# Optimization experiments

Hardware: AMD Instinct MI355X
Metric: run time of the kernel (lower is better)

The kernel has to match this reference:

```python
import jax, jax.numpy as jnp
import numpy as np

LR = 0.001  # fixed self.lr in ODE_Vanilla

B, T, I, H, C = 128, 256, 256, 1024, 10


def setup_inputs() -> dict:
    key = jax.random.key(0)
    ks = jax.random.split(key, 6)
    stdv = 1.0 / np.sqrt(H)
    u = lambda k, shape: jax.random.uniform(k, shape, jnp.float32, -stdv, stdv)
    return {
        "X": jax.random.normal(ks[0], (B, T, I), jnp.float32),
        "hidden": jnp.zeros((B, H), jnp.float32),
        "alpha": jnp.zeros((1,), jnp.float32),  # alpha is excluded from re-init, stays 0.0
        "b": u(ks[1], (H,)),
        "Wh": u(ks[2], (H, H)),
        "Wx": u(ks[3], (I, H)),
        "fc_w": u(ks[4], (H, C)),
        "fc_b": u(ks[5], (C,)),
    }


def reference(X, hidden, alpha, b, Wh, Wx, fc_w, fc_b):
    # X: (B, T, I) -> scan over time-major (T, B, I)
    a = alpha[0]
    Xt = jnp.transpose(X, (1, 0, 2))

    def step(h, x):
        # phi = relu(h @ Wh + x @ Wx + b)
        phi = jax.nn.relu(h @ Wh + x @ Wx + b)
        mask = (phi > 0).astype(h.dtype)
        # st = a*I - diag(mask) @ Wh; grad = st @ (a*h - phi)
        # collapses to: a*v - mask * (v @ Wh^T), with v = a*h - phi
        v = a * h - phi
        grad = a * v - mask * (v @ Wh.T)
        h_new = h - LR * grad
        return h_new, h_new

    h_final, outs = jax.lax.scan(step, hidden, Xt)  # outs: (T, B, H)
    # last_layer (single_output=False, class task): FC over all timesteps
    out = jnp.transpose(outs, (1, 0, 2)) @ fc_w + fc_b  # (B, T, C)
    return out.reshape(-1, out.shape[-1]), h_final
```

## Files before the change

### kernel.cpp

```cpp
#include <hip/hip_runtime.h>


constexpr int Bsz = 128, Tn = 256, In = 256, Hn = 1024, Cn = 10;
constexpr float LR = 0.001f;

__global__ __launch_bounds__(256) void k_transpose(const float* __restrict__ W,
                                                   float* __restrict__ WT) {
  __shared__ float tile[32][33];
  const int bx = blockIdx.x * 32, by = blockIdx.y * 32;
  const int tx = threadIdx.x & 31, ty = threadIdx.x >> 5;
#pragma unroll
  for (int dy = 0; dy < 32; dy += 8)
    tile[ty + dy][tx] = W[(size_t)(by + ty + dy) * Hn + bx + tx];
  __syncthreads();
#pragma unroll
  for (int dy = 0; dy < 32; dy += 8)
    WT[(size_t)(bx + ty + dy) * Hn + by + tx] = tile[tx][ty + dy];
}

__global__ __launch_bounds__(256) void k_init(float* __restrict__ out,
                                              const float* __restrict__ fc_b,
                                              float* __restrict__ h_cur,
                                              const float* __restrict__ hidden) {
  const int i = blockIdx.x * blockDim.x + threadIdx.x;
  if (i < Bsz * Tn * Cn) out[i] = fc_b[i % Cn];
  if (i < Bsz * Hn) h_cur[i] = hidden[i];
}

__device__ __forceinline__ void fma4(float4& a, float s, const float4& w) {
  a.x = fmaf(s, w.x, a.x);
  a.y = fmaf(s, w.y, a.y);
  a.z = fmaf(s, w.z, a.z);
  a.w = fmaf(s, w.w, a.w);
}

__device__ __forceinline__ float4 shfl4(float4 v, int m) {
  v.x = __shfl_xor(v.x, m, 64);
  v.y = __shfl_xor(v.y, m, 64);
  v.z = __shfl_xor(v.z, m, 64);
  v.w = __shfl_xor(v.w, m, 64);
  return v;
}

__device__ __forceinline__ float4 add4(float4 a, float4 b) {
  return make_float4(a.x + b.x, a.y + b.y, a.z + b.z, a.w + b.w);
}

__global__ __launch_bounds__(256) void k_xw(const float* __restrict__ X,
                                            const float* __restrict__ Wx,
                                            const float* __restrict__ bias,
                                            float* __restrict__ xw) {
  const int nt = blockIdx.x & 15, mt = blockIdx.x >> 4;
  const int t = mt >> 1, b0 = (mt & 1) * 64;
  const int cl = threadIdx.x & 15, rg = threadIdx.x >> 4;
  const int col = nt * 64 + cl * 4;
  const int row = b0 + rg * 4;
  float4 acc0 = {0, 0, 0, 0}, acc1 = {0, 0, 0, 0}, acc2 = {0, 0, 0, 0},
         acc3 = {0, 0, 0, 0};
  const size_t xstride = (size_t)Tn * In;
  const float* xp = X + ((size_t)row * Tn + t) * In;
  const float* wp = Wx + col;
#pragma unroll 2
  for (int k = 0; k < In; k += 4) {
    const float4 x0 = *(const float4*)(xp + k);
    const float4 x1 = *(const float4*)(xp + xstride + k);
    const float4 x2 = *(const float4*)(xp + 2 * xstride + k);
    const float4 x3 = *(const float4*)(xp + 3 * xstride + k);
    const float4 w0 = *(const float4*)(wp + (size_t)k * Hn);
    const float4 w1 = *(const float4*)(wp + (size_t)(k + 1) * Hn);
    const float4 w2 = *(const float4*)(wp + (size_t)(k + 2) * Hn);
    const float4 w3 = *(const float4*)(wp + (size_t)(k + 3) * Hn);
    fma4(acc0, x0.x, w0); fma4(acc0, x0.y, w1); fma4(acc0, x0.z, w2); fma4(acc0, x0.w, w3);
    fma4(acc1, x1.x, w0); fma4(acc1, x1.y, w1); fma4(acc1, x1.z, w2); fma4(acc1, x1.w, w3);
    fma4(acc2, x2.x, w0); fma4(acc2, x2.y, w1); fma4(acc2, x2.z, w2); fma4(acc2, x2.w, w3);
    fma4(acc3, x3.x, w0); fma4(acc3, x3.y, w1); fma4(acc3, x3.z, w2); fma4(acc3, x3.w, w3);
  }
  const float4 b4 = *(const float4*)(bias + col);
  float4 o[4] = {acc0, acc1, acc2, acc3};
#pragma unroll
  for (int i = 0; i < 4; i++) {
    float4 v = o[i];
    v.x += b4.x; v.y += b4.y; v.z += b4.z; v.w += b4.w;
    *(float4*)(xw + ((size_t)t * Bsz + row + i) * Hn + col) = v;
  }
}

__device__ __forceinline__ void gemm8g(const float* __restrict__ rows,
                                       const float* __restrict__ W, int kk,
                                       int col, float4 acc[8]) {
#pragma unroll
  for (int q = 0; q < 4; q++) {
    const int k = 4 * kk + 256 * q;
    const float* Wp = W + (size_t)k * Hn + col;
    const float4 w0 = *(const float4*)(Wp);
    const float4 w1 = *(const float4*)(Wp + Hn);
    const float4 w2 = *(const float4*)(Wp + 2 * Hn);
    const float4 w3 = *(const float4*)(Wp + 3 * Hn);
#pragma unroll
    for (int r = 0; r < 8; r++) {
      const float4 h4 = *(const float4*)(rows + (size_t)r * Hn + k);
      fma4(acc[r], h4.x, w0);
      fma4(acc[r], h4.y, w1);
      fma4(acc[r], h4.z, w2);
      fma4(acc[r], h4.w, w3);
    }
  }
}

__device__ __forceinline__ void reduce_vs(float4 acc[8], int c4, int ksw,
                                          int wv, float (*part)[8][16]) {
  const bool u1 = ksw & 1;
#pragma unroll
  for (int i = 0; i < 4; i++) {
    const float4 snd = u1 ? acc[i] : acc[i + 4];
    const float4 kp = u1 ? acc[i + 4] : acc[i];
    acc[i] = add4(kp, shfl4(snd, 4));
  }
  const bool u2 = ksw & 2;
#pragma unroll
  for (int i = 0; i < 2; i++) {
    const float4 snd = u2 ? acc[i] : acc[i + 2];
    const float4 kp = u2 ? acc[i + 2] : acc[i];
    acc[i] = add4(kp, shfl4(snd, 8));
  }
  const bool u3 = ksw & 4;
  {
    const float4 snd = u3 ? acc[0] : acc[1];
    const float4 kp = u3 ? acc[1] : acc[0];
    acc[0] = add4(kp, shfl4(snd, 16));
  }
  const bool u4 = ksw & 8;
  float sx = u4 ? acc[0].x : acc[0].z;
  float sy = u4 ? acc[0].y : acc[0].w;
  const float kx = u4 ? acc[0].z : acc[0].x;
  const float ky = u4 ? acc[0].w : acc[0].y;
  sx = __shfl_xor(sx, 32, 64);
  sy = __shfl_xor(sy, 32, 64);
  const int r_own = ((ksw & 1) << 2) | (ksw & 2) | ((ksw >> 2) & 1);
  const int c_own = 4 * c4 + (u4 ? 2 : 0);
  *(float2*)&part[wv][r_own][c_own] = make_float2(kx + sx, ky + sy);
}

template <int PRE>
__global__ __launch_bounds__(256, 4) void k_phase1(
    const float* __restrict__ h, const float* __restrict__ X,
    const float* __restrict__ Wh, const float* __restrict__ Wx,
    const float* __restrict__ bias, const float* __restrict__ alpha,
    const float* __restrict__ xw, float* __restrict__ v_out, int t) {
  __shared__ float part[4][8][16];
  const int ct = blockIdx.x & 63, rt = blockIdx.x >> 6;
  const int c0 = ct * 16, r0 = rt * 8;
  const int tid = threadIdx.x;
  const int c4 = tid & 3, kk = tid >> 2;
  const int col = c0 + 4 * c4;
  const int wv = tid >> 6, ksw = (tid & 63) >> 2;
  const float* hbase = h + (size_t)r0 * Hn;

  float4 acc[8];
#pragma unroll
  for (int r = 0; r < 8; r++) acc[r] = {0.f, 0.f, 0.f, 0.f};
  gemm8g(hbase, Wh, kk, col, acc);
  if (!PRE) {
    const int kx = 4 * kk;
    const float* Wp = Wx + (size_t)kx * Hn + col;
    const float4 w0 = *(const float4*)(Wp);
    const float4 w1 = *(const float4*)(Wp + Hn);
    const float4 w2 = *(const float4*)(Wp + 2 * Hn);
    const float4 w3 = *(const float4*)(Wp + 3 * Hn);
#pragma unroll
    for (int r = 0; r < 8; r++) {
      const float4 x4 =
          *(const float4*)(X + ((size_t)(r0 + r) * Tn + t) * In + kx);
      fma4(acc[r], x4.x, w0);
      fma4(acc[r], x4.y, w1);
      fma4(acc[r], x4.z, w2);
      fma4(acc[r], x4.w, w3);
    }
  }
  reduce_vs(acc, c4, ksw, wv, part);
  __syncthreads();
  if (tid < 128) {
    const int r = tid >> 4, c = tid & 15;
    const float u =
        part[0][r][c] + part[1][r][c] + part[2][r][c] + part[3][r][c];
    const float a1 =
        PRE ? xw[((size_t)t * Bsz + r0 + r) * Hn + c0 + c] : bias[c0 + c];
    const float av = alpha[0];
    const float hv = hbase[(size_t)r * Hn + c0 + c];
    v_out[(size_t)(r0 + r) * Hn + c0 + c] = av * hv - fmaxf(u + a1, 0.f);
  }
}

__global__ __launch_bounds__(256, 4) void k_phase2(
    float* __restrict__ h, const float* __restrict__ v_in,
    const float* __restrict__ WT, const float* __restrict__ alpha,
    const float* __restrict__ fc_w, float* __restrict__ out,
    float* __restrict__ hfin, int t, int last) {
  __shared__ float part[4][8][16];
  __shared__ float hn_s[8][16];
  const int ct = blockIdx.x & 63, rt = blockIdx.x >> 6;
  const int c0 = ct * 16, r0 = rt * 8;
  const int tid = threadIdx.x;
  const int c4 = tid & 3, kk = tid >> 2;
  const int col = c0 + 4 * c4;
  const int wv = tid >> 6, ksw = (tid & 63) >> 2;
  const float* vbase = v_in + (size_t)r0 * Hn;

  float4 acc[8];
#pragma unroll
  for (int r = 0; r < 8; r++) acc[r] = {0.f, 0.f, 0.f, 0.f};
  gemm8g(vbase, WT, kk, col, acc);
  reduce_vs(acc, c4, ksw, wv, part);
  __syncthreads();
  if (tid < 128) {
    const int r = tid >> 4, c = tid & 15;
    const float u =
        part[0][r][c] + part[1][r][c] + part[2][r][c] + part[3][r][c];
    const float av = alpha[0];
    const size_t hoff = (size_t)(r0 + r) * Hn + c0 + c;
    const float vv = vbase[(size_t)r * Hn + c0 + c];
    const float hv = h[hoff];
    const float hn = hv - LR * (av * vv - ((av * hv - vv) > 0.f ? u : 0.f));
    h[hoff] = hn;
    if (last) hfin[hoff] = hn;
    hn_s[r][c] = hn;
  }
  __syncthreads();
  if (tid < 80) {
    const int rr = tid / 10, c = tid % 10;
    float s = 0.f;
#pragma unroll
    for (int jj = 0; jj < 16; jj++)
      s += hn_s[rr][jj] * fc_w[(size_t)(c0 + jj) * Cn + c];
    atomicAdd(&out[((size_t)(r0 + rr) * Tn + t) * Cn + c], s);
  }
}

extern "C" void kernel_launch(void* const* d_in, const int* in_sizes, int n_in,
                              void* d_out, int out_size, void* d_ws, size_t ws_size,
                              hipStream_t stream) {
  const float* X      = (const float*)d_in[0];
  const float* hidden = (const float*)d_in[1];
  const float* alpha  = (const float*)d_in[2];
  const float* bias   = (const float*)d_in[3];
  const float* Wh     = (const float*)d_in[4];
  const float* Wx     = (const float*)d_in[5];
  const float* fc_w   = (const float*)d_in[6];
  const float* fc_b   = (const float*)d_in[7];
  float* out  = (float*)d_out;
  float* hfin = out + (size_t)Bsz * Tn * Cn;

  char* ws = (char*)d_ws;
  float* WhT   = (float*)ws;
  float* h_cur = WhT + (size_t)Hn * Hn;
  float* v_buf = h_cur + (size_t)Bsz * Hn;
  float* XW    = v_buf + (size_t)Bsz * Hn;
  const size_t need =
      ((size_t)Hn * Hn + 2 * (size_t)Bsz * Hn + (size_t)Bsz * Tn * Hn) *
      sizeof(float);
  const bool pre = ws_size >= need;

  k_transpose<<<dim3(32, 32), 256, 0, stream>>>(Wh, WhT);
  k_init<<<(Bsz * Tn * Cn + 255) / 256, 256, 0, stream>>>(out, fc_b, h_cur,
                                                          hidden);
  if (pre) k_xw<<<8192, 256, 0, stream>>>(X, Wx, bias, XW);
  for (int t = 0; t < Tn; t++) {
    if (pre)
      k_phase1<1><<<1024, 256, 0, stream>>>(h_cur, X, Wh, Wx, bias, alpha, XW,
                                            v_buf, t);
    else
      k_phase1<0><<<1024, 256, 0, stream>>>(h_cur, X, Wh, Wx, bias, alpha, XW,
                                            v_buf, t);
    k_phase2<<<1024, 256, 0, stream>>>(h_cur, v_buf, WhT, alpha, fc_w, out,
                                       hfin, t, t == Tn - 1);
  }
}
```

Baseline: 6.030 ms.

## Move FC projection into extra phase1 blocks for previous timestep, drop atomics

The per-timestep FC output projection is removed from the tail of phase2, where it added a sync and atomicAdds. It now runs in 16 extra blocks of the next step's phase1 launch, which read the previous h_cur and write the output directly with the bias added. A final small kernel handles the last timestep, and the init kernel no longer fills the output with the bias. This shortens phase2's critical path and removes atomic contention, at the cost of some imbalance from the extra phase1 blocks.

```diff
diff --git a/kernel.cpp b/kernel.cpp
--- a/kernel.cpp
+++ b/kernel.cpp
@@ -18,13 +18,10 @@
     WT[(size_t)(bx + ty + dy) * Hn + by + tx] = tile[tx][ty + dy];
 }
 
-__global__ __launch_bounds__(256) void k_init(float* __restrict__ out,
-                                              const float* __restrict__ fc_b,
-                                              float* __restrict__ h_cur,
+__global__ __launch_bounds__(256) void k_init(float* __restrict__ h_cur,
                                               const float* __restrict__ hidden) {
-  const int i = blockIdx.x * blockDim.x + threadIdx.x;
-  if (i < Bsz * Tn * Cn) out[i] = fc_b[i % Cn];
-  if (i < Bsz * Hn) h_cur[i] = hidden[i];
+  const int i = blockIdx.x * 256 + threadIdx.x;
+  h_cur[i] = hidden[i];
 }
 
 __device__ __forceinline__ void fma4(float4& a, float s, const float4& w) {
@@ -146,11 +143,36 @@
     const float* __restrict__ h, const float* __restrict__ X,
     const float* __restrict__ Wh, const float* __restrict__ Wx,
     const float* __restrict__ bias, const float* __restrict__ alpha,
-    const float* __restrict__ xw, float* __restrict__ v_out, int t) {
+    const float* __restrict__ xw, const float* __restrict__ fc_w,
+    const float* __restrict__ fc_b, float* __restrict__ out,
+    float* __restrict__ v_out, int t) {
+  const int tid = threadIdx.x;
+  if (blockIdx.x >= 1024) {
+    if (t == 0) return;
+    const int r0b = (blockIdx.x - 1024) * 8;
+    const int r = tid >> 5, l = tid & 31;
+    const int c = l & 15, half = l >> 4;
+    float s = 0.f;
+    if (c < Cn) {
+      const float* hp = h + (size_t)(r0b + r) * Hn + half * 512;
+#pragma unroll 4
+      for (int k = 0; k < 512; k += 4) {
+        const float4 h4 = *(const float4*)(hp + k);
+        const float* fw = fc_w + (size_t)(half * 512 + k) * Cn + c;
+        s = fmaf(h4.x, fw[0], s);
+        s = fmaf(h4.y, fw[Cn], s);
+        s = fmaf(h4.z, fw[2 * Cn], s);
+        s = fmaf(h4.w, fw[3 * Cn], s);
+      }
+    }
+    s += __shfl_xor(s, 16, 64);
+    if (c < Cn && half == 0)
+      out[((size_t)(r0b + r) * Tn + (t - 1)) * Cn + c] = s + fc_b[c];
+    return;
+  }
   __shared__ float part[4][8][16];
   const int ct = blockIdx.x & 63, rt = blockIdx.x >> 6;
   const int c0 = ct * 16, r0 = rt * 8;
-  const int tid = threadIdx.x;
   const int c4 = tid & 3, kk = tid >> 2;
   const int col = c0 + 4 * c4;
   const int wv = tid >> 6, ksw = (tid & 63) >> 2;
@@ -194,10 +216,8 @@
 __global__ __launch_bounds__(256, 4) void k_phase2(
     float* __restrict__ h, const float* __restrict__ v_in,
     const float* __restrict__ WT, const float* __restrict__ alpha,
-    const float* __restrict__ fc_w, float* __restrict__ out,
-    float* __restrict__ hfin, int t, int last) {
+    float* __restrict__ hfin, int last) {
   __shared__ float part[4][8][16];
-  __shared__ float hn_s[8][16];
   const int ct = blockIdx.x & 63, rt = blockIdx.x >> 6;
   const int c0 = ct * 16, r0 = rt * 8;
   const int tid = threadIdx.x;
@@ -223,17 +243,32 @@
     const float hn = hv - LR * (av * vv - ((av * hv - vv) > 0.f ? u : 0.f));
     h[hoff] = hn;
     if (last) hfin[hoff] = hn;
-    hn_s[r][c] = hn;
-  }
-  __syncthreads();
-  if (tid < 80) {
-    const int rr = tid / 10, c = tid % 10;
-    float s = 0.f;
-#pragma unroll
-    for (int jj = 0; jj < 16; jj++)
-      s += hn_s[rr][jj] * fc_w[(size_t)(c0 + jj) * Cn + c];
-    atomicAdd(&out[((size_t)(r0 + rr) * Tn + t) * Cn + c], s);
-  }
+  }
+}
+
+__global__ __launch_bounds__(256) void k_fc_last(const float* __restrict__ h,
+                                                 const float* __restrict__ fc_w,
+                                                 const float* __restrict__ fc_b,
+                                                 float* __restrict__ out) {
+  const int r0 = blockIdx.x * 8;
+  const int r = threadIdx.x >> 5, l = threadIdx.x & 31;
+  const int c = l & 15, half = l >> 4;
+  float s = 0.f;
+  if (c < Cn) {
+    const float* hp = h + (size_t)(r0 + r) * Hn + half * 512;
+#pragma unroll 4
+    for (int k = 0; k < 512; k += 4) {
+      const float4 h4 = *(const float4*)(hp + k);
+      const float* fw = fc_w + (size_t)(half * 512 + k) * Cn + c;
+      s = fmaf(h4.x, fw[0], s);
+      s = fmaf(h4.y, fw[Cn], s);
+      s = fmaf(h4.z, fw[2 * Cn], s);
+      s = fmaf(h4.w, fw[3 * Cn], s);
+    }
+  }
+  s += __shfl_xor(s, 16, 64);
+  if (c < Cn && half == 0)
+    out[((size_t)(r0 + r) * Tn + (Tn - 1)) * Cn + c] = s + fc_b[c];
 }
 
 extern "C" void kernel_launch(void* const* d_in, const int* in_sizes, int n_in,
@@ -261,17 +296,17 @@
   const bool pre = ws_size >= need;
 
   k_transpose<<<dim3(32, 32), 256, 0, stream>>>(Wh, WhT);
-  k_init<<<(Bsz * Tn * Cn + 255) / 256, 256, 0, stream>>>(out, fc_b, h_cur,
-                                                          hidden);
+  k_init<<<512, 256, 0, stream>>>(h_cur, hidden);
   if (pre) k_xw<<<8192, 256, 0, stream>>>(X, Wx, bias, XW);
   for (int t = 0; t < Tn; t++) {
     if (pre)
-      k_phase1<1><<<1024, 256, 0, stream>>>(h_cur, X, Wh, Wx, bias, alpha, XW,
-                                            v_buf, t);
+      k_phase1<1><<<1040, 256, 0, stream>>>(h_cur, X, Wh, Wx, bias, alpha, XW,
+                                            fc_w, fc_b, out, v_buf, t);
     else
-      k_phase1<0><<<1024, 256, 0, stream>>>(h_cur, X, Wh, Wx, bias, alpha, XW,
-                                            v_buf, t);
-    k_phase2<<<1024, 256, 0, stream>>>(h_cur, v_buf, WhT, alpha, fc_w, out,
-                                       hfin, t, t == Tn - 1);
-  }
-}
+      k_phase1<0><<<1040, 256, 0, stream>>>(h_cur, X, Wh, Wx, bias, alpha, XW,
+                                            fc_w, fc_b, out, v_buf, t);
+    k_phase2<<<1024, 256, 0, stream>>>(h_cur, v_buf, WhT, alpha, hfin,
+                                       t == Tn - 1);
+  }
+  k_fc_last<<<16, 256, 0, stream>>>(h_cur, fc_w, fc_b, out);
+}
```

After: 7.036 ms. +16.7%, slower.

## Enlarge recurrent GEMM tiles to 16 rows with 512-thread blocks

Applied to the files above, without the earlier changes.

Each per-step phase kernel now computes a 16-row by 16-column output tile with 512 threads instead of an 8x16 tile with 256 threads. Every weight float4 loaded is reused across twice as many batch rows, which halves total weight traffic per timestep and halves the block count. The cross-lane reduction is reworked to fit the larger accumulator array, and the epilogue loads of h, v and xw are hoisted above the GEMM so their latency overlaps it. In exchange, each thread holds 16 float4 accumulators, which raises register pressure and may lower occupancy. Only 512 blocks run per launch.

```diff
diff --git a/kernel.cpp b/kernel.cpp
--- a/kernel.cpp
+++ b/kernel.cpp
@@ -85,19 +85,19 @@
   }
 }
 
-__device__ __forceinline__ void gemm8g(const float* __restrict__ rows,
-                                       const float* __restrict__ W, int kk,
-                                       int col, float4 acc[8]) {
-#pragma unroll
-  for (int q = 0; q < 4; q++) {
-    const int k = 4 * kk + 256 * q;
+__device__ __forceinline__ void gemm16g(const float* __restrict__ rows,
+                                        const float* __restrict__ W, int kk,
+                                        int col, float4 acc[16]) {
+#pragma unroll
+  for (int q = 0; q < 2; q++) {
+    const int k = 4 * kk + 512 * q;
     const float* Wp = W + (size_t)k * Hn + col;
     const float4 w0 = *(const float4*)(Wp);
     const float4 w1 = *(const float4*)(Wp + Hn);
     const float4 w2 = *(const float4*)(Wp + 2 * Hn);
     const float4 w3 = *(const float4*)(Wp + 3 * Hn);
 #pragma unroll
-    for (int r = 0; r < 8; r++) {
+    for (int r = 0; r < 16; r++) {
       const float4 h4 = *(const float4*)(rows + (size_t)r * Hn + k);
       fma4(acc[r], h4.x, w0);
       fma4(acc[r], h4.y, w1);
@@ -107,126 +107,132 @@
   }
 }
 
-__device__ __forceinline__ void reduce_vs(float4 acc[8], int c4, int ksw,
-                                          int wv, float (*part)[8][16]) {
+__device__ __forceinline__ void reduce_vs16(float4 acc[16], int c4, int ksw,
+                                            int wv, float (*part)[16][20]) {
   const bool u1 = ksw & 1;
 #pragma unroll
+  for (int i = 0; i < 8; i++) {
+    const float4 snd = u1 ? acc[i] : acc[i + 8];
+    const float4 kp = u1 ? acc[i + 8] : acc[i];
+    acc[i] = add4(kp, shfl4(snd, 4));
+  }
+  const bool u2 = ksw & 2;
+#pragma unroll
   for (int i = 0; i < 4; i++) {
-    const float4 snd = u1 ? acc[i] : acc[i + 4];
-    const float4 kp = u1 ? acc[i + 4] : acc[i];
-    acc[i] = add4(kp, shfl4(snd, 4));
-  }
-  const bool u2 = ksw & 2;
+    const float4 snd = u2 ? acc[i] : acc[i + 4];
+    const float4 kp = u2 ? acc[i + 4] : acc[i];
+    acc[i] = add4(kp, shfl4(snd, 8));
+  }
+  const bool u3 = ksw & 4;
 #pragma unroll
   for (int i = 0; i < 2; i++) {
-    const float4 snd = u2 ? acc[i] : acc[i + 2];
-    const float4 kp = u2 ? acc[i + 2] : acc[i];
-    acc[i] = add4(kp, shfl4(snd, 8));
-  }
-  const bool u3 = ksw & 4;
+    const float4 snd = u3 ? acc[i] : acc[i + 2];
+    const float4 kp = u3 ? acc[i + 2] : acc[i];
+    acc[i] = add4(kp, shfl4(snd, 16));
+  }
+  const bool u4 = ksw & 8;
   {
-    const float4 snd = u3 ? acc[0] : acc[1];
-    const float4 kp = u3 ? acc[1] : acc[0];
-    acc[0] = add4(kp, shfl4(snd, 16));
-  }
-  const bool u4 = ksw & 8;
-  float sx = u4 ? acc[0].x : acc[0].z;
-  float sy = u4 ? acc[0].y : acc[0].w;
-  const float kx = u4 ? acc[0].z : acc[0].x;
-  const float ky = u4 ? acc[0].w : acc[0].y;
-  sx = __shfl_xor(sx, 32, 64);
-  sy = __shfl_xor(sy, 32, 64);
-  const int r_own = ((ksw & 1) << 2) | (ksw & 2) | ((ksw >> 2) & 1);
-  const int c_own = 4 * c4 + (u4 ? 2 : 0);
-  *(float2*)&part[wv][r_own][c_own] = make_float2(kx + sx, ky + sy);
+    const float4 snd = u4 ? acc[0] : acc[1];
+    const float4 kp = u4 ? acc[1] : acc[0];
+    acc[0] = add4(kp, shfl4(snd, 32));
+  }
+  const int r_own = (u1 ? 8 : 0) | (u2 ? 4 : 0) | (u3 ? 2 : 0) | (u4 ? 1 : 0);
+  *(float4*)&part[wv][r_own][4 * c4] = acc[0];
 }
 
 template <int PRE>
-__global__ __launch_bounds__(256, 4) void k_phase1(
+__global__ __launch_bounds__(512, 4) void k_phase1(
     const float* __restrict__ h, const float* __restrict__ X,
     const float* __restrict__ Wh, const float* __restrict__ Wx,
     const float* __restrict__ bias, const float* __restrict__ alpha,
     const float* __restrict__ xw, float* __restrict__ v_out, int t) {
-  __shared__ float part[4][8][16];
+  __shared__ float part[8][16][20];
   const int ct = blockIdx.x & 63, rt = blockIdx.x >> 6;
-  const int c0 = ct * 16, r0 = rt * 8;
+  const int c0 = ct * 16, r0 = rt * 16;
   const int tid = threadIdx.x;
   const int c4 = tid & 3, kk = tid >> 2;
   const int col = c0 + 4 * c4;
-  const int wv = tid >> 6, ksw = (tid & 63) >> 2;
+  const int wv = tid >> 6, ksw = (tid >> 2) & 15;
   const float* hbase = h + (size_t)r0 * Hn;
 
-  float4 acc[8];
-#pragma unroll
-  for (int r = 0; r < 8; r++) acc[r] = {0.f, 0.f, 0.f, 0.f};
-  gemm8g(hbase, Wh, kk, col, acc);
+  float a1 = 0.f, hv = 0.f;
+  if (tid < 256) {
+    const int r = tid >> 4, c = tid & 15;
+    a1 = PRE ? xw[((size_t)t * Bsz + r0 + r) * Hn + c0 + c] : bias[c0 + c];
+    hv = hbase[(size_t)r * Hn + c0 + c];
+  }
+
+  float4 acc[16];
+#pragma unroll
+  for (int r = 0; r < 16; r++) acc[r] = {0.f, 0.f, 0.f, 0.f};
+  gemm16g(hbase, Wh, kk, col, acc);
   if (!PRE) {
-    const int kx = 4 * kk;
+    const int kx = 2 * kk;
     const float* Wp = Wx + (size_t)kx * Hn + col;
-    const float4 w0 = *(const float4*)(Wp);
-    const float4 w1 = *(const float4*)(Wp + Hn);
-    const float4 w2 = *(const float4*)(Wp + 2 * Hn);
-    const float4 w3 = *(const float4*)(Wp + 3 * Hn);
-#pragma unroll
-    for (int r = 0; r < 8; r++) {
-      const float4 x4 =
-          *(const float4*)(X + ((size_t)(r0 + r) * Tn + t) * In + kx);
-      fma4(acc[r], x4.x, w0);
-      fma4(acc[r], x4.y, w1);
-      fma4(acc[r], x4.z, w2);
-      fma4(acc[r], x4.w, w3);
+    const float4 wa = *(const float4*)(Wp);
+    const float4 wb = *(const float4*)(Wp + Hn);
+#pragma unroll
+    for (int r = 0; r < 16; r++) {
+      const float2 x2 =
+          *(const float2*)(X + ((size_t)(r0 + r) * Tn + t) * In + kx);
+      fma4(acc[r], x2.x, wa);
+      fma4(acc[r], x2.y, wb);
     }
   }
-  reduce_vs(acc, c4, ksw, wv, part);
-  __syncthreads();
-  if (tid < 128) {
-    const int r = tid >> 4, c = tid & 15;
-    const float u =
-        part[0][r][c] + part[1][r][c] + part[2][r][c] + part[3][r][c];
-    const float a1 =
-        PRE ? xw[((size_t)t * Bsz + r0 + r) * Hn + c0 + c] : bias[c0 + c];
+  reduce_vs16(acc, c4, ksw, wv, part);
+  __syncthreads();
+  if (tid < 256) {
+    const int r = tid >> 4, c = tid & 15;
+    float u = part[0][r][c];
+#pragma unroll
+    for (int w = 1; w < 8; w++) u += part[w][r][c];
     const float av = alpha[0];
-    const float hv = hbase[(size_t)r * Hn + c0 + c];
     v_out[(size_t)(r0 + r) * Hn + c0 + c] = av * hv - fmaxf(u + a1, 0.f);
   }
 }
 
-__global__ __launch_bounds__(256, 4) void k_phase2(
+__global__ __launch_bounds__(512, 4) void k_phase2(
     float* __restrict__ h, const float* __restrict__ v_in,
     const float* __restrict__ WT, const float* __restrict__ alpha,
     const float* __restrict__ fc_w, float* __restrict__ out,
     float* __restrict__ hfin, int t, int last) {
-  __shared__ float part[4][8][16];
-  __shared__ float hn_s[8][16];
+  __shared__ float part[8][16][20];
+  __shared__ float hn_s[16][16];
   const int ct = blockIdx.x & 63, rt = blockIdx.x >> 6;
-  const int c0 = ct * 16, r0 = rt * 8;
+  const int c0 = ct * 16, r0 = rt * 16;
   const int tid = threadIdx.x;
   const int c4 = tid & 3, kk = tid >> 2;
   const int col = c0 + 4 * c4;
-  const int wv = tid >> 6, ksw = (tid & 63) >> 2;
+  const int wv = tid >> 6, ksw = (tid >> 2) & 15;
   const float* vbase = v_in + (size_t)r0 * Hn;
 
-  float4 acc[8];
-#pragma unroll
-  for (int r = 0; r < 8; r++) acc[r] = {0.f, 0.f, 0.f, 0.f};
-  gemm8g(vbase, WT, kk, col, acc);
-  reduce_vs(acc, c4, ksw, wv, part);
-  __syncthreads();
-  if (tid < 128) {
-    const int r = tid >> 4, c = tid & 15;
-    const float u =
-        part[0][r][c] + part[1][r][c] + part[2][r][c] + part[3][r][c];
+  float hv = 0.f, vv = 0.f;
+  if (tid < 256) {
+    const int r = tid >> 4, c = tid & 15;
+    hv = h[(size_t)(r0 + r) * Hn + c0 + c];
+    vv = vbase[(size_t)r * Hn + c0 + c];
+  }
+
+  float4 acc[16];
+#pragma unroll
+  for (int r = 0; r < 16; r++) acc[r] = {0.f, 0.f, 0.f, 0.f};
+  gemm16g(vbase, WT, kk, col, acc);
+  reduce_vs16(acc, c4, ksw, wv, part);
+  __syncthreads();
+  if (tid < 256) {
+    const int r = tid >> 4, c = tid & 15;
+    float u = part[0][r][c];
+#pragma unroll
+    for (int w = 1; w < 8; w++) u += part[w][r][c];
     const float av = alpha[0];
     const size_t hoff = (size_t)(r0 + r) * Hn + c0 + c;
-    const float vv = vbase[(size_t)r * Hn + c0 + c];
-    const float hv = h[hoff];
     const float hn = hv - LR * (av * vv - ((av * hv - vv) > 0.f ? u : 0.f));
     h[hoff] = hn;
     if (last) hfin[hoff] = hn;
     hn_s[r][c] = hn;
   }
   __syncthreads();
-  if (tid < 80) {
+  if (tid < 160) {
     const int rr = tid / 10, c = tid % 10;
     float s = 0.f;
 #pragma unroll
@@ -266,12 +272,12 @@
   if (pre) k_xw<<<8192, 256, 0, stream>>>(X, Wx, bias, XW);
   for (int t = 0; t < Tn; t++) {
     if (pre)
-      k_phase1<1><<<1024, 256, 0, stream>>>(h_cur, X, Wh, Wx, bias, alpha, XW,
-                                            v_buf, t);
+      k_phase1<1><<<512, 512, 0, stream>>>(h_cur, X, Wh, Wx, bias, alpha, XW,
+                                           v_buf, t);
     else
-      k_phase1<0><<<1024, 256, 0, stream>>>(h_cur, X, Wh, Wx, bias, alpha, XW,
-                                            v_buf, t);
-    k_phase2<<<1024, 256, 0, stream>>>(h_cur, v_buf, WhT, alpha, fc_w, out,
-                                       hfin, t, t == Tn - 1);
-  }
-}
+      k_phase1<0><<<512, 512, 0, stream>>>(h_cur, X, Wh, Wx, bias, alpha, XW,
+                                           v_buf, t);
+    k_phase2<<<512, 512, 0, stream>>>(h_cur, v_buf, WhT, alpha, fc_w, out,
+                                      hfin, t, t == Tn - 1);
+  }
+}
```

New measurement: 16.52 ms. +173.9%, slower.

## Use nontemporal weight loads and shuffle-reduce the FC projection in phase2

Applied to the files above, without the earlier changes.

Weight loads for Wh, WT and Wx switch to nontemporal vector loads, meant to keep the streamed weights from evicting the reused h/v rows from cache. The per-step FC epilogue drops the shared-memory staging and the extra __syncthreads: each of the 128 threads forms 10 partial products and reduces them across its 16-lane group with xor shuffles. One lane per row then issues 10 atomics, replacing the 80-thread loop. Alpha is also loaded earlier. The risk is that nontemporal hints can hurt if the weights would otherwise stay resident in L2/MALL across timesteps, since they are reused every step.

```diff
diff --git a/kernel.cpp b/kernel.cpp
--- a/kernel.cpp
+++ b/kernel.cpp
@@ -3,6 +3,8 @@
 
 constexpr int Bsz = 128, Tn = 256, In = 256, Hn = 1024, Cn = 10;
 constexpr float LR = 0.001f;
+
+typedef float f4 __attribute__((ext_vector_type(4)));
 
 __global__ __launch_bounds__(256) void k_transpose(const float* __restrict__ W,
                                                    float* __restrict__ WT) {
@@ -32,6 +34,17 @@
   a.y = fmaf(s, w.y, a.y);
   a.z = fmaf(s, w.z, a.z);
   a.w = fmaf(s, w.w, a.w);
+}
+
+__device__ __forceinline__ void fma4v(float4& a, float s, const f4& w) {
+  a.x = fmaf(s, w.x, a.x);
+  a.y = fmaf(s, w.y, a.y);
+  a.z = fmaf(s, w.z, a.z);
+  a.w = fmaf(s, w.w, a.w);
+}
+
+__device__ __forceinline__ f4 ldnt(const float* p) {
+  return __builtin_nontemporal_load((const f4*)p);
 }
 
 __device__ __forceinline__ float4 shfl4(float4 v, int m) {
@@ -92,17 +105,17 @@
   for (int q = 0; q < 4; q++) {
     const int k = 4 * kk + 256 * q;
     const float* Wp = W + (size_t)k * Hn + col;
-    const float4 w0 = *(const float4*)(Wp);
-    const float4 w1 = *(const float4*)(Wp + Hn);
-    const float4 w2 = *(const float4*)(Wp + 2 * Hn);
-    const float4 w3 = *(const float4*)(Wp + 3 * Hn);
+    const f4 w0 = ldnt(Wp);
+    const f4 w1 = ldnt(Wp + Hn);
+    const f4 w2 = ldnt(Wp + 2 * Hn);
+    const f4 w3 = ldnt(Wp + 3 * Hn);
 #pragma unroll
     for (int r = 0; r < 8; r++) {
       const float4 h4 = *(const float4*)(rows + (size_t)r * Hn + k);
-      fma4(acc[r], h4.x, w0);
-      fma4(acc[r], h4.y, w1);
-      fma4(acc[r], h4.z, w2);
-      fma4(acc[r], h4.w, w3);
+      fma4v(acc[r], h4.x, w0);
+      fma4v(acc[r], h4.y, w1);
+      fma4v(acc[r], h4.z, w2);
+      fma4v(acc[r], h4.w, w3);
     }
   }
 }
@@ -155,6 +168,7 @@
   const int col = c0 + 4 * c4;
   const int wv = tid >> 6, ksw = (tid & 63) >> 2;
   const float* hbase = h + (size_t)r0 * Hn;
+  const float av = alpha[0];
 
   float4 acc[8];
 #pragma unroll
@@ -163,18 +177,18 @@
   if (!PRE) {
     const int kx = 4 * kk;
     const float* Wp = Wx + (size_t)kx * Hn + col;
-    const float4 w0 = *(const float4*)(Wp);
-    const float4 w1 = *(const float4*)(Wp + Hn);
-    const float4 w2 = *(const float4*)(Wp + 2 * Hn);
-    const float4 w3 = *(const float4*)(Wp + 3 * Hn);
+    const f4 w0 = ldnt(Wp);
+    const f4 w1 = ldnt(Wp + Hn);
+    const f4 w2 = ldnt(Wp + 2 * Hn);
+    const f4 w3 = ldnt(Wp + 3 * Hn);
 #pragma unroll
     for (int r = 0; r < 8; r++) {
       const float4 x4 =
           *(const float4*)(X + ((size_t)(r0 + r) * Tn + t) * In + kx);
-      fma4(acc[r], x4.x, w0);
-      fma4(acc[r], x4.y, w1);
-      fma4(acc[r], x4.z, w2);
-      fma4(acc[r], x4.w, w3);
+      fma4v(acc[r], x4.x, w0);
+      fma4v(acc[r], x4.y, w1);
+      fma4v(acc[r], x4.z, w2);
+      fma4v(acc[r], x4.w, w3);
     }
   }
   reduce_vs(acc, c4, ksw, wv, part);
@@ -185,7 +199,6 @@
         part[0][r][c] + part[1][r][c] + part[2][r][c] + part[3][r][c];
     const float a1 =
         PRE ? xw[((size_t)t * Bsz + r0 + r) * Hn + c0 + c] : bias[c0 + c];
-    const float av = alpha[0];
     const float hv = hbase[(size_t)r * Hn + c0 + c];
     v_out[(size_t)(r0 + r) * Hn + c0 + c] = av * hv - fmaxf(u + a1, 0.f);
   }
@@ -197,7 +210,6 @@
     const float* __restrict__ fc_w, float* __restrict__ out,
     float* __restrict__ hfin, int t, int last) {
   __shared__ float part[4][8][16];
-  __shared__ float hn_s[8][16];
   const int ct = blockIdx.x & 63, rt = blockIdx.x >> 6;
   const int c0 = ct * 16, r0 = rt * 8;
   const int tid = threadIdx.x;
@@ -205,6 +217,7 @@
   const int col = c0 + 4 * c4;
   const int wv = tid >> 6, ksw = (tid & 63) >> 2;
   const float* vbase = v_in + (size_t)r0 * Hn;
+  const float av = alpha[0];
 
   float4 acc[8];
 #pragma unroll
@@ -216,23 +229,25 @@
     const int r = tid >> 4, c = tid & 15;
     const float u =
         part[0][r][c] + part[1][r][c] + part[2][r][c] + part[3][r][c];
-    const float av = alpha[0];
     const size_t hoff = (size_t)(r0 + r) * Hn + c0 + c;
     const float vv = vbase[(size_t)r * Hn + c0 + c];
     const float hv = h[hoff];
     const float hn = hv - LR * (av * vv - ((av * hv - vv) > 0.f ? u : 0.f));
     h[hoff] = hn;
     if (last) hfin[hoff] = hn;
-    hn_s[r][c] = hn;
-  }
-  __syncthreads();
-  if (tid < 80) {
-    const int rr = tid / 10, c = tid % 10;
-    float s = 0.f;
-#pragma unroll
-    for (int jj = 0; jj < 16; jj++)
-      s += hn_s[rr][jj] * fc_w[(size_t)(c0 + jj) * Cn + c];
-    atomicAdd(&out[((size_t)(r0 + rr) * Tn + t) * Cn + c], s);
+    float p[Cn];
+    const float* fw = fc_w + (size_t)(c0 + c) * Cn;
+#pragma unroll
+    for (int cc = 0; cc < Cn; cc++) p[cc] = hn * fw[cc];
+#pragma unroll
+    for (int m = 1; m <= 8; m <<= 1)
+#pragma unroll
+      for (int cc = 0; cc < Cn; cc++) p[cc] += __shfl_xor(p[cc], m, 64);
+    if (c == 0) {
+      float* op = out + ((size_t)(r0 + r) * Tn + t) * Cn;
+#pragma unroll
+      for (int cc = 0; cc < Cn; cc++) atomicAdd(op + cc, p[cc]);
+    }
   }
 }
 
```

New measurement: 10.81 ms. 1.79x slower.
